# Performance work log

Measured on AMD Instinct MI355X. Metric: run time of the kernel, lower is better.

The kernel has to match this reference:

```python
import jax, jax.numpy as jnp
import numpy as np

DIM = 1024
HEADS = 16
HEAD_DIM = DIM // HEADS
HIDDEN = 4 * DIM
EPS = 1e-5

def _layernorm(x, w, b):
    mu = jnp.mean(x, axis=-1, keepdims=True)
    var = jnp.mean(jnp.square(x - mu), axis=-1, keepdims=True)
    return (x - mu) * jax.lax.rsqrt(var + EPS) * w + b

def setup_inputs() -> dict:
    key = jax.random.key(0)
    ks = jax.random.split(key, 8)
    B, N, C = 4, 1024, DIM
    s = lambda fan_in: 1.0 / np.sqrt(fan_in)
    return {
        "x": jax.random.normal(ks[0], (B, N, C), dtype=jnp.float32),
        "ln1_w": jnp.ones((C,), jnp.float32),
        "ln1_b": jnp.zeros((C,), jnp.float32),
        "qkv_w": jax.random.normal(ks[1], (3 * C, C), jnp.float32) * s(C),
        "proj_w": jax.random.normal(ks[2], (C, C), jnp.float32) * s(C),
        "proj_b": jnp.zeros((C,), jnp.float32),
        "ln2_w": jnp.ones((C,), jnp.float32),
        "ln2_b": jnp.zeros((C,), jnp.float32),
        "fc1_w": jax.random.normal(ks[3], (HIDDEN, C), jnp.float32) * s(C),
        "fc1_b": jnp.zeros((HIDDEN,), jnp.float32),
        "fc2_w": jax.random.normal(ks[4], (C, HIDDEN), jnp.float32) * s(HIDDEN),
        "fc2_b": jnp.zeros((C,), jnp.float32),
    }

def reference(x, ln1_w, ln1_b, qkv_w, proj_w, proj_b, ln2_w, ln2_b, fc1_w, fc1_b, fc2_w, fc2_b):
    B, N, C = x.shape
    H, D = HEADS, HEAD_DIM
    scale = D ** -0.5
    # --- attention branch (pre-norm) ---
    h = _layernorm(x, ln1_w, ln1_b)
    qkv = jnp.einsum('bnc,oc->bno', h, qkv_w)          # [B,N,3C], no bias (qkv_bias=False)
    qkv = qkv.reshape(B, N, 3, H, D)
    q = jnp.transpose(qkv[:, :, 0], (0, 2, 1, 3))       # [B,H,N,D]
    k = jnp.transpose(qkv[:, :, 1], (0, 2, 1, 3))
    v = jnp.transpose(qkv[:, :, 2], (0, 2, 1, 3))
    attn = jnp.einsum('bhnd,bhmd->bhnm', q, k) * scale  # [B,H,N,N]
    attn = jax.nn.softmax(attn, axis=-1)
    o = jnp.einsum('bhnm,bhmd->bhnd', attn, v)          # [B,H,N,D]
    o = jnp.transpose(o, (0, 2, 1, 3)).reshape(B, N, C)
    o = jnp.einsum('bnc,oc->bno', o, proj_w) + proj_b
    x = x + o
    # --- MLP branch (pre-norm); drop=0.0 -> identity ---
    h = _layernorm(x, ln2_w, ln2_b)
    h = jnp.einsum('bnc,hc->bnh', h, fc1_w) + fc1_b
    h = jax.nn.gelu(h, approximate=False)               # nn.GELU exact erf form
    h = jnp.einsum('bnh,ch->bnc', h, fc2_w) + fc2_b
    return x + h
```

## Files before the change

### kernel.cpp

```cpp
#include <hip/hip_runtime.h>
#include <hip/hip_bf16.h>
#include <math.h>
#include <stdint.h>

#define SEQ 1024
#define CDIM 1024
#define NHEAD 16
#define HIDDEN 4096
#define BATCH 4
#define MROWS (BATCH*SEQ)

using bf16x8 = __attribute__((ext_vector_type(8))) short;
using f32x4  = __attribute__((ext_vector_type(4))) float;

__device__ __forceinline__ short f2bf(float f) {
    union { float f; uint32_t u; } c; c.f = f;
    const uint32_t u = c.u + 0x7FFFu + ((c.u >> 16) & 1u);
    return (short)(u >> 16);
}

__device__ __forceinline__ float gelu_exact(float v) {
    return 0.5f * v * (1.0f + erff(v * 0.70710678118654752440f));
}

__device__ __forceinline__ void gload_lds16(const short* g, short* lds) {
    __builtin_amdgcn_global_load_lds(
        (const __attribute__((address_space(1))) void*)(uintptr_t)g,
        (__attribute__((address_space(3))) void*)(uintptr_t)lds,
        16, 0, 0);
}

__global__ void cvt_bf16_kernel(const float* __restrict__ in, short* __restrict__ out) {
    const size_t i = ((size_t)blockIdx.x * 256 + threadIdx.x) * 8;
    const float4 a = *(const float4*)(in + i);
    const float4 b = *(const float4*)(in + i + 4);
    bf16x8 s;
    s[0] = f2bf(a.x); s[1] = f2bf(a.y); s[2] = f2bf(a.z); s[3] = f2bf(a.w);
    s[4] = f2bf(b.x); s[5] = f2bf(b.y); s[6] = f2bf(b.z); s[7] = f2bf(b.w);
    *(bf16x8*)(out + i) = s;
}

__global__ void ln_kernel(const float* __restrict__ x, const float* __restrict__ w,
                          const float* __restrict__ b, short* __restrict__ out) {
    const int row = blockIdx.x;
    const int t = threadIdx.x;
    const float4* xr = (const float4*)(x + (size_t)row * CDIM);
    float4 v = xr[t];
    float s  = v.x + v.y + v.z + v.w;
    float sq = v.x*v.x + v.y*v.y + v.z*v.z + v.w*v.w;
    #pragma unroll
    for (int off = 32; off; off >>= 1) {
        s  += __shfl_down(s, off);
        sq += __shfl_down(sq, off);
    }
    __shared__ float ss[4], ssq[4];
    const int wid = t >> 6, lane = t & 63;
    if (lane == 0) { ss[wid] = s; ssq[wid] = sq; }
    __syncthreads();
    s  = ss[0] + ss[1] + ss[2] + ss[3];
    sq = ssq[0] + ssq[1] + ssq[2] + ssq[3];
    const float mu  = s * (1.0f / CDIM);
    const float var = sq * (1.0f / CDIM) - mu * mu;
    const float rs  = rsqrtf(var + 1e-5f);
    const float4 wv = ((const float4*)w)[t];
    const float4 bv = ((const float4*)b)[t];
    short4 o;
    o.x = f2bf((v.x - mu) * rs * wv.x + bv.x);
    o.y = f2bf((v.y - mu) * rs * wv.y + bv.y);
    o.z = f2bf((v.z - mu) * rs * wv.z + bv.z);
    o.w = f2bf((v.w - mu) * rs * wv.w + bv.w);
    *(short4*)(out + (size_t)row * CDIM + t * 4) = o;
}

template<int BN, bool BIAS, bool RES, bool GELU_, bool OUTBF16>
__global__ __launch_bounds__(256) void mgemm(
    const short* __restrict__ A, const short* __restrict__ B,
    const float* __restrict__ bias, const float* __restrict__ res,
    void* __restrict__ Cv, int M, int N, int K)
{
    constexpr int MF = (BN == 128) ? 4 : 2;
    __shared__ __align__(16) short As[3][128 * 32];
    __shared__ __align__(16) short Bs[3][BN * 32];
    const int t = threadIdx.x;
    const int w = t >> 6, l = t & 63;

    const int gx = gridDim.x;
    const int nwg = gx * gridDim.y;
    const int lid = blockIdx.y * gx + blockIdx.x;
    const int swz = (lid & 7) * (nwg >> 3) + (lid >> 3);
    const int bx = swz % gx, by = swz / gx;
    const int m0 = by * 128, n0 = bx * BN;

    const int wrow = (BN == 128) ? (w >> 1) * 64 : w * 32;
    const int wcol = (BN == 128) ? (w & 1) * 64 : 0;

    const short* agp0 = A + (size_t)(m0 + w * 32 + (l >> 2)) * K + (l & 3) * 8;
    const short* agp1 = agp0 + (size_t)16 * K;
    const short* bgp0;
    const short* bgp1 = nullptr;
    if (BN == 128) {
        bgp0 = B + (size_t)(n0 + w * 32 + (l >> 2)) * K + (l & 3) * 8;
        bgp1 = bgp0 + (size_t)16 * K;
    } else {
        bgp0 = B + (size_t)(n0 + w * 16 + (l >> 2)) * K + (l & 3) * 8;
    }

    int aoff[MF], boff[4];
    #pragma unroll
    for (int m = 0; m < MF; ++m) aoff[m] = (wrow + m * 16 + (l & 15)) * 32 + (l >> 4) * 8;
    #pragma unroll
    for (int n = 0; n < 4; ++n)  boff[n] = (wcol + n * 16 + (l & 15)) * 32 + (l >> 4) * 8;

    auto stage = [&](int k0, int buf) {
        short* ldsA = &As[buf][w * 1024];
        gload_lds16(agp0 + k0, ldsA);
        gload_lds16(agp1 + k0, ldsA + 512);
        if (BN == 128) {
            short* ldsB = &Bs[buf][w * 1024];
            gload_lds16(bgp0 + k0, ldsB);
            gload_lds16(bgp1 + k0, ldsB + 512);
        } else {
            gload_lds16(bgp0 + k0, &Bs[buf][w * 512]);
        }
    };

    f32x4 acc[MF][4] = {};
    const int T = K / 32;
    stage(0, 0);
    stage(32, 1);
    int cur = 0;
    for (int kt = 0; kt < T; ++kt) {
        if (kt < T - 1) {
            if constexpr (BN == 128) asm volatile("s_waitcnt vmcnt(4)" ::: "memory");
            else                     asm volatile("s_waitcnt vmcnt(3)" ::: "memory");
        } else {
            asm volatile("s_waitcnt vmcnt(0)" ::: "memory");
        }
        __builtin_amdgcn_sched_barrier(0);
        __builtin_amdgcn_s_barrier();
        __builtin_amdgcn_sched_barrier(0);
        if (kt + 2 < T) {
            int nb = kt + 2; nb -= (nb >= 3) ? ((nb / 3) * 3) : 0;
            stage((kt + 2) * 32, nb);
        }
        bf16x8 af[MF], bfr[4];
        #pragma unroll
        for (int m = 0; m < MF; ++m) af[m]  = *(const bf16x8*)&As[cur][aoff[m]];
        #pragma unroll
        for (int n = 0; n < 4; ++n)  bfr[n] = *(const bf16x8*)&Bs[cur][boff[n]];
        #pragma unroll
        for (int m = 0; m < MF; ++m)
            #pragma unroll
            for (int n = 0; n < 4; ++n)
                acc[m][n] = __builtin_amdgcn_mfma_f32_16x16x32_bf16(af[m], bfr[n], acc[m][n], 0, 0, 0);
        cur = (cur == 2) ? 0 : cur + 1;
    }

    const int lr4 = (l >> 4) * 4, lc = l & 15;
    #pragma unroll
    for (int m = 0; m < MF; ++m) {
        #pragma unroll
        for (int n = 0; n < 4; ++n) {
            const int col = n0 + wcol + n * 16 + lc;
            const float bv = BIAS ? bias[col] : 0.0f;
            #pragma unroll
            for (int r = 0; r < 4; ++r) {
                const int row = m0 + wrow + m * 16 + lr4 + r;
                float v = acc[m][n][r] + bv;
                if (GELU_) v = gelu_exact(v);
                if (RES)   v += res[(size_t)row * N + col];
                if (OUTBF16) ((short*)Cv)[(size_t)row * N + col] = f2bf(v);
                else         ((float*)Cv)[(size_t)row * N + col] = v;
            }
        }
    }
}

__global__ __launch_bounds__(256) void qkv_gemm(
    const short* __restrict__ A, const short* __restrict__ B,
    short* __restrict__ qkvb, short* __restrict__ VT, int K)
{
    __shared__ __align__(16) short As[3][128 * 32];
    __shared__ __align__(16) short Bs[3][128 * 32];
    const int t = threadIdx.x;
    const int w = t >> 6, l = t & 63;
    const int wr = w >> 1, wc = w & 1;

    const int gx = gridDim.x;
    const int nwg = gx * gridDim.y;
    const int lid = blockIdx.y * gx + blockIdx.x;
    const int swz = (lid & 7) * (nwg >> 3) + (lid >> 3);
    const int bx = swz % gx, by = swz / gx;
    const int m0 = by * 128, n0 = bx * 128;

    const short* agp0 = A + (size_t)(m0 + w * 32 + (l >> 2)) * K + (l & 3) * 8;
    const short* agp1 = agp0 + (size_t)16 * K;
    const short* bgp0 = B + (size_t)(n0 + w * 32 + (l >> 2)) * K + (l & 3) * 8;
    const short* bgp1 = bgp0 + (size_t)16 * K;

    int aoff[4], boff[4];
    #pragma unroll
    for (int m = 0; m < 4; ++m) aoff[m] = (wr * 64 + m * 16 + (l & 15)) * 32 + (l >> 4) * 8;
    #pragma unroll
    for (int n = 0; n < 4; ++n) boff[n] = (wc * 64 + n * 16 + (l & 15)) * 32 + (l >> 4) * 8;

    auto stage = [&](int k0, int buf) {
        short* ldsA = &As[buf][w * 1024];
        short* ldsB = &Bs[buf][w * 1024];
        gload_lds16(agp0 + k0, ldsA);
        gload_lds16(agp1 + k0, ldsA + 512);
        gload_lds16(bgp0 + k0, ldsB);
        gload_lds16(bgp1 + k0, ldsB + 512);
    };

    f32x4 acc[4][4] = {};
    const int T = K / 32;
    stage(0, 0);
    stage(32, 1);
    int cur = 0;
    for (int kt = 0; kt < T; ++kt) {
        if (kt < T - 1) asm volatile("s_waitcnt vmcnt(4)" ::: "memory");
        else            asm volatile("s_waitcnt vmcnt(0)" ::: "memory");
        __builtin_amdgcn_sched_barrier(0);
        __builtin_amdgcn_s_barrier();
        __builtin_amdgcn_sched_barrier(0);
        if (kt + 2 < T) {
            int nb = kt + 2; nb -= (nb >= 3) ? ((nb / 3) * 3) : 0;
            stage((kt + 2) * 32, nb);
        }
        bf16x8 af[4], bfr[4];
        #pragma unroll
        for (int m = 0; m < 4; ++m) af[m]  = *(const bf16x8*)&As[cur][aoff[m]];
        #pragma unroll
        for (int n = 0; n < 4; ++n) bfr[n] = *(const bf16x8*)&Bs[cur][boff[n]];
        #pragma unroll
        for (int m = 0; m < 4; ++m)
            #pragma unroll
            for (int n = 0; n < 4; ++n)
                acc[m][n] = __builtin_amdgcn_mfma_f32_16x16x32_bf16(af[m], bfr[n], acc[m][n], 0, 0, 0);
        cur = (cur == 2) ? 0 : cur + 1;
    }

    const int lr4 = (l >> 4) * 4, lc = l & 15;
    if (n0 < 2048) {
        const float sc = (n0 < 1024) ? 0.125f : 1.0f;
        #pragma unroll
        for (int m = 0; m < 4; ++m) {
            #pragma unroll
            for (int n = 0; n < 4; ++n) {
                const int col = n0 + wc * 64 + n * 16 + lc;
                #pragma unroll
                for (int r = 0; r < 4; ++r) {
                    const int row = m0 + wr * 64 + m * 16 + lr4 + r;
                    qkvb[(size_t)row * 2048 + col] = f2bf(acc[m][n][r] * sc);
                }
            }
        }
    } else {
        #pragma unroll
        for (int m = 0; m < 4; ++m) {
            const int row0 = m0 + wr * 64 + m * 16 + lr4;
            const int b = row0 >> 10, nseq = row0 & 1023;
            #pragma unroll
            for (int n = 0; n < 4; ++n) {
                const int c2 = n0 - 2048 + wc * 64 + n * 16 + lc;
                const int h = c2 >> 6, d = c2 & 63;
                short4 v4;
                v4.x = f2bf(acc[m][n][0]); v4.y = f2bf(acc[m][n][1]);
                v4.z = f2bf(acc[m][n][2]); v4.w = f2bf(acc[m][n][3]);
                *(short4*)&VT[(((size_t)(b * 16 + h) * 64 + d) * 1024) + nseq] = v4;
            }
        }
    }
}

__global__ __launch_bounds__(256) void fattn(const short* __restrict__ qkvb,
                                             const short* __restrict__ VT,
                                             short* __restrict__ o) {
    const int bh = blockIdx.y;
    const int b = bh >> 4, h = bh & 15;
    const int q0 = blockIdx.x * 64;
    const int t = threadIdx.x, w = t >> 6, l = t & 63;

    __shared__ __align__(16) short Ks[2][64 * 64];
    __shared__ __align__(16) short Vs[2][64 * 64];
    __shared__ __align__(16) short Ps[4][1024];

    const size_t qrow = (size_t)(b * SEQ + q0 + w * 16 + (l & 15)) * 2048 + h * 64;
    bf16x8 qf[2];
    qf[0] = *(const bf16x8*)&qkvb[qrow + (l >> 4) * 8];
    qf[1] = *(const bf16x8*)&qkvb[qrow + 32 + (l >> 4) * 8];

    const int srow = l >> 3;
    const int sc16 = (l & 7) ^ (srow & 7);
    const short* Kg = qkvb + 1024 + h * 64;
    const short* Vg = VT + (size_t)bh * 64 * 1024;

    f32x4 acc[4] = {};
    float mrow[4] = {-1e30f, -1e30f, -1e30f, -1e30f};
    float lrow[4] = {0.f, 0.f, 0.f, 0.f};

    auto stage = [&](int kt, int buf) {
        const int kv0 = kt * 64;
        #pragma unroll
        for (int i = 0; i < 2; ++i) {
            const int r0 = w * 16 + i * 8;
            gload_lds16(Kg + (size_t)(b * SEQ + kv0 + r0 + srow) * 2048 + sc16 * 8,
                        &Ks[buf][r0 * 64]);
            gload_lds16(Vg + (size_t)(r0 + srow) * 1024 + kv0 + sc16 * 8,
                        &Vs[buf][r0 * 64]);
        }
    };

    stage(0, 0);
    for (int kt = 0; kt < 16; ++kt) {
        const int cur = kt & 1;
        __syncthreads();
        if (kt + 1 < 16) stage(kt + 1, cur ^ 1);

        f32x4 sacc[4];
        #pragma unroll
        for (int nt = 0; nt < 4; ++nt) {
            f32x4 z = {};
            #pragma unroll
            for (int ks = 0; ks < 2; ++ks) {
                const int row = nt * 16 + (l & 15);
                const int c16 = (ks * 4 + (l >> 4)) ^ (row & 7);
                const bf16x8 kf = *(const bf16x8*)&Ks[cur][row * 64 + c16 * 8];
                z = __builtin_amdgcn_mfma_f32_16x16x32_bf16(qf[ks], kf, z, 0, 0, 0);
            }
            sacc[nt] = z;
        }
        float tmax[4], tsum[4], fac[4];
        #pragma unroll
        for (int r = 0; r < 4; ++r)
            tmax[r] = fmaxf(fmaxf(sacc[0][r], sacc[1][r]), fmaxf(sacc[2][r], sacc[3][r]));
        #pragma unroll
        for (int off = 1; off <= 8; off <<= 1)
            #pragma unroll
            for (int r = 0; r < 4; ++r)
                tmax[r] = fmaxf(tmax[r], __shfl_xor(tmax[r], off));
        #pragma unroll
        for (int r = 0; r < 4; ++r) {
            const float nm = fmaxf(mrow[r], tmax[r]);
            fac[r] = __expf(mrow[r] - nm);
            mrow[r] = nm;
            tsum[r] = 0.0f;
        }
        #pragma unroll
        for (int nt = 0; nt < 4; ++nt) {
            #pragma unroll
            for (int r = 0; r < 4; ++r) {
                const float p = __expf(sacc[nt][r] - mrow[r]);
                tsum[r] += p;
                const int q = (l >> 4) * 4 + r;
                const int kv = nt * 16 + (l & 15);
                union { float f; uint32_t u; } cu; cu.f = p;
                Ps[w][q * 64 + (kv ^ ((q & 7) << 3))] = (short)((cu.u + 0x8000u) >> 16);
            }
        }
        #pragma unroll
        for (int off = 1; off <= 8; off <<= 1)
            #pragma unroll
            for (int r = 0; r < 4; ++r)
                tsum[r] += __shfl_xor(tsum[r], off);
        #pragma unroll
        for (int r = 0; r < 4; ++r) lrow[r] = lrow[r] * fac[r] + tsum[r];
        #pragma unroll
        for (int nt2 = 0; nt2 < 4; ++nt2)
            #pragma unroll
            for (int r = 0; r < 4; ++r)
                acc[nt2][r] *= fac[r];
        #pragma unroll
        for (int ks = 0; ks < 2; ++ks) {
            const int ql = l & 15;
            const bf16x8 pa = *(const bf16x8*)&Ps[w][ql * 64 + ((ks * 32 + (l >> 4) * 8) ^ ((ql & 7) << 3))];
            #pragma unroll
            for (int nt2 = 0; nt2 < 4; ++nt2) {
                const int row = nt2 * 16 + (l & 15);
                const int c16 = (ks * 4 + (l >> 4)) ^ (row & 7);
                const bf16x8 vf = *(const bf16x8*)&Vs[cur][row * 64 + c16 * 8];
                acc[nt2] = __builtin_amdgcn_mfma_f32_16x16x32_bf16(pa, vf, acc[nt2], 0, 0, 0);
            }
        }
    }
    #pragma unroll
    for (int r = 0; r < 4; ++r) {
        const float rcp = 1.0f / lrow[r];
        const int q = q0 + w * 16 + (l >> 4) * 4 + r;
        #pragma unroll
        for (int nt2 = 0; nt2 < 4; ++nt2) {
            const int d = nt2 * 16 + (l & 15);
            o[(size_t)(b * SEQ + q) * CDIM + h * 64 + d] = f2bf(acc[nt2][r] * rcp);
        }
    }
}

extern "C" void kernel_launch(void* const* d_in, const int* in_sizes, int n_in,
                              void* d_out, int out_size, void* d_ws, size_t ws_size,
                              hipStream_t stream) {
    const float* x      = (const float*)d_in[0];
    const float* ln1_w  = (const float*)d_in[1];
    const float* ln1_b  = (const float*)d_in[2];
    const float* qkv_w  = (const float*)d_in[3];
    const float* proj_w = (const float*)d_in[4];
    const float* proj_b = (const float*)d_in[5];
    const float* ln2_w  = (const float*)d_in[6];
    const float* ln2_b  = (const float*)d_in[7];
    const float* fc1_w  = (const float*)d_in[8];
    const float* fc1_b  = (const float*)d_in[9];
    const float* fc2_w  = (const float*)d_in[10];
    const float* fc2_b  = (const float*)d_in[11];
    float* out = (float*)d_out;

    short* ws16  = (short*)d_ws;
    short* wqkv  = ws16;
    short* wproj = ws16 + 3145728;
    short* wfc1  = ws16 + 4194304;
    short* wfc2  = ws16 + 8388608;
    char*  wsb   = (char*)d_ws;
    short* qkvb  = (short*)(wsb + (size_t)24 * 1024 * 1024);
    short* VT    = (short*)(wsb + (size_t)40 * 1024 * 1024);
    short* mlp1  = (short*)(wsb + (size_t)24 * 1024 * 1024);
    short* hbuf  = (short*)(wsb + (size_t)72 * 1024 * 1024);

    cvt_bf16_kernel<<<1536, 256, 0, stream>>>(qkv_w, wqkv);
    cvt_bf16_kernel<<< 512, 256, 0, stream>>>(proj_w, wproj);
    cvt_bf16_kernel<<<2048, 256, 0, stream>>>(fc1_w, wfc1);
    cvt_bf16_kernel<<<2048, 256, 0, stream>>>(fc2_w, wfc2);

    ln_kernel<<<MROWS, 256, 0, stream>>>(x, ln1_w, ln1_b, hbuf);
    qkv_gemm<<<dim3(24, 32), 256, 0, stream>>>(hbuf, wqkv, qkvb, VT, 1024);
    fattn<<<dim3(SEQ / 64, BATCH * NHEAD), 256, 0, stream>>>(qkvb, VT, hbuf);
    mgemm<64,true,true,false,false><<<dim3(16, 32), 256, 0, stream>>>(
        hbuf, wproj, proj_b, x, out, MROWS, 1024, 1024);
    ln_kernel<<<MROWS, 256, 0, stream>>>(out, ln2_w, ln2_b, hbuf);
    mgemm<128,true,false,true,true><<<dim3(32, 32), 256, 0, stream>>>(
        hbuf, wfc1, fc1_b, nullptr, mlp1, MROWS, 4096, 1024);
    mgemm<64,true,true,false,false><<<dim3(16, 32), 256, 0, stream>>>(
        mlp1, wfc2, fc2_b, out, out, MROWS, 1024, 4096);
}
```

Measured before the change: 252.1 us.

## Add 256x256 8-wave ping-pong GEMM for fc1 and XOR-swizzle LDS layouts

```diff
diff --git a/kernel.cpp b/kernel.cpp
--- a/kernel.cpp
+++ b/kernel.cpp
@@ -72,6 +72,142 @@
     *(short4*)(out + (size_t)row * CDIM + t * 4) = o;
 }
 
+template<bool BIAS, bool RES, bool GELU_, bool OUTBF16>
+__global__ __launch_bounds__(512) void gemm8p(
+    const short* __restrict__ A, const short* __restrict__ B,
+    const float* __restrict__ bias, const float* __restrict__ res,
+    void* __restrict__ Cv, int M, int N, int K)
+{
+    __shared__ __align__(16) short As[2][256 * 64];
+    __shared__ __align__(16) short Bs[2][256 * 64];
+    const int t = threadIdx.x;
+    const int w = t >> 6, l = t & 63;
+    const int wm = w >> 2, wn = w & 3;
+
+    const int lid = blockIdx.y * gridDim.x + blockIdx.x;
+    const int xcd = lid & 7, c = lid >> 3;
+    const int by = (xcd >> 1) * 4 + (c >> 3);
+    const int bx = (xcd & 1) * 8 + (c & 7);
+    const int m0 = by * 256, n0 = bx * 256;
+
+    const int trow = t >> 3;
+    const int k8s = ((t & 7) ^ (trow & 7)) * 8;
+    const short* Ag = A + (size_t)(m0 + trow) * K + k8s;
+    const short* Bg = B + (size_t)(n0 + trow) * K + k8s;
+
+    const int fr = l & 15, g = l >> 4;
+    const int sw = fr & 7;
+    const int ak0 = (g ^ sw) * 8;
+    const int ak1 = ((4 + g) ^ sw) * 8;
+    int aoff[8], boff[4];
+    #pragma unroll
+    for (int mf = 0; mf < 8; ++mf) aoff[mf] = (wm * 128 + mf * 16 + fr) * 64;
+    #pragma unroll
+    for (int nf = 0; nf < 4; ++nf) boff[nf] = (wn * 64 + nf * 16 + fr) * 64;
+
+    f32x4 acc[8][4] = {};
+
+#define STAGE8(Gb, LDSb, kt, h)                                             \
+    {                                                                       \
+        gload_lds16((Gb) + (size_t)((h) * 128) * K + (kt) * 64,             \
+                    (LDSb) + ((h) * 128 + w * 8) * 64);                     \
+        gload_lds16((Gb) + (size_t)((h) * 128 + 64) * K + (kt) * 64,        \
+                    (LDSb) + ((h) * 128 + 64 + w * 8) * 64);                \
+    }
+
+    STAGE8(Ag, As[0], 0, 0); STAGE8(Ag, As[0], 0, 1);
+    STAGE8(Bg, Bs[0], 0, 0); STAGE8(Bg, Bs[0], 0, 1);
+    asm volatile("s_waitcnt vmcnt(0)" ::: "memory");
+    __builtin_amdgcn_s_barrier();
+
+    const int T = K / 64;
+    for (int kt = 0; kt < T; ++kt) {
+        short* curA = &As[kt & 1][0];
+        short* curB = &Bs[kt & 1][0];
+        short* nxtA = &As[(kt & 1) ^ 1][0];
+        short* nxtB = &Bs[(kt & 1) ^ 1][0];
+        const bool pre = (kt + 1 < T);
+        bf16x8 bfr[4], af[4];
+
+        if (pre) STAGE8(Ag, nxtA, kt + 1, 0);
+        #pragma unroll
+        for (int nf = 0; nf < 4; ++nf) bfr[nf] = *(const bf16x8*)&curB[boff[nf] + ak0];
+        #pragma unroll
+        for (int mf = 0; mf < 4; ++mf) af[mf] = *(const bf16x8*)&curA[aoff[mf] + ak0];
+        __builtin_amdgcn_s_barrier();
+        __builtin_amdgcn_s_setprio(1);
+        #pragma unroll
+        for (int mf = 0; mf < 4; ++mf)
+            #pragma unroll
+            for (int nf = 0; nf < 4; ++nf)
+                acc[mf][nf] = __builtin_amdgcn_mfma_f32_16x16x32_bf16(af[mf], bfr[nf], acc[mf][nf], 0, 0, 0);
+        __builtin_amdgcn_s_setprio(0);
+        __builtin_amdgcn_s_barrier();
+
+        if (pre) STAGE8(Ag, nxtA, kt + 1, 1);
+        #pragma unroll
+        for (int mf = 0; mf < 4; ++mf) af[mf] = *(const bf16x8*)&curA[aoff[4 + mf] + ak0];
+        __builtin_amdgcn_s_barrier();
+        __builtin_amdgcn_s_setprio(1);
+        #pragma unroll
+        for (int mf = 0; mf < 4; ++mf)
+            #pragma unroll
+            for (int nf = 0; nf < 4; ++nf)
+                acc[4 + mf][nf] = __builtin_amdgcn_mfma_f32_16x16x32_bf16(af[mf], bfr[nf], acc[4 + mf][nf], 0, 0, 0);
+        __builtin_amdgcn_s_setprio(0);
+        __builtin_amdgcn_s_barrier();
+
+        if (pre) STAGE8(Bg, nxtB, kt + 1, 0);
+        #pragma unroll
+        for (int nf = 0; nf < 4; ++nf) bfr[nf] = *(const bf16x8*)&curB[boff[nf] + ak1];
+        #pragma unroll
+        for (int mf = 0; mf < 4; ++mf) af[mf] = *(const bf16x8*)&curA[aoff[mf] + ak1];
+        __builtin_amdgcn_s_barrier();
+        __builtin_amdgcn_s_setprio(1);
+        #pragma unroll
+        for (int mf = 0; mf < 4; ++mf)
+            #pragma unroll
+            for (int nf = 0; nf < 4; ++nf)
+                acc[mf][nf] = __builtin_amdgcn_mfma_f32_16x16x32_bf16(af[mf], bfr[nf], acc[mf][nf], 0, 0, 0);
+        __builtin_amdgcn_s_setprio(0);
+        __builtin_amdgcn_s_barrier();
+
+        if (pre) STAGE8(Bg, nxtB, kt + 1, 1);
+        #pragma unroll
+        for (int mf = 0; mf < 4; ++mf) af[mf] = *(const bf16x8*)&curA[aoff[4 + mf] + ak1];
+        __builtin_amdgcn_s_barrier();
+        __builtin_amdgcn_s_setprio(1);
+        #pragma unroll
+        for (int mf = 0; mf < 4; ++mf)
+            #pragma unroll
+            for (int nf = 0; nf < 4; ++nf)
+                acc[4 + mf][nf] = __builtin_amdgcn_mfma_f32_16x16x32_bf16(af[mf], bfr[nf], acc[4 + mf][nf], 0, 0, 0);
+        __builtin_amdgcn_s_setprio(0);
+        asm volatile("s_waitcnt vmcnt(0)" ::: "memory");
+        __builtin_amdgcn_s_barrier();
+    }
+#undef STAGE8
+
+    const int lr4 = (l >> 4) * 4, lc = l & 15;
+    #pragma unroll
+    for (int mf = 0; mf < 8; ++mf) {
+        #pragma unroll
+        for (int nf = 0; nf < 4; ++nf) {
+            const int col = n0 + wn * 64 + nf * 16 + lc;
+            const float bv = BIAS ? bias[col] : 0.0f;
+            #pragma unroll
+            for (int r = 0; r < 4; ++r) {
+                const int row = m0 + wm * 128 + mf * 16 + lr4 + r;
+                float v = acc[mf][nf][r] + bv;
+                if (GELU_) v = gelu_exact(v);
+                if (RES)   v += res[(size_t)row * N + col];
+                if (OUTBF16) ((short*)Cv)[(size_t)row * N + col] = f2bf(v);
+                else         ((float*)Cv)[(size_t)row * N + col] = v;
+            }
+        }
+    }
+}
+
 template<int BN, bool BIAS, bool RES, bool GELU_, bool OUTBF16>
 __global__ __launch_bounds__(256) void mgemm(
     const short* __restrict__ A, const short* __restrict__ B,
@@ -87,29 +223,32 @@
     const int gx = gridDim.x;
     const int nwg = gx * gridDim.y;
     const int lid = blockIdx.y * gx + blockIdx.x;
-    const int swz = (lid & 7) * (nwg >> 3) + (lid >> 3);
-    const int bx = swz % gx, by = swz / gx;
+    const int swzb = (lid & 7) * (nwg >> 3) + (lid >> 3);
+    const int bx = swzb % gx, by = swzb / gx;
     const int m0 = by * 128, n0 = bx * BN;
 
     const int wrow = (BN == 128) ? (w >> 1) * 64 : w * 32;
     const int wcol = (BN == 128) ? (w & 1) * 64 : 0;
 
-    const short* agp0 = A + (size_t)(m0 + w * 32 + (l >> 2)) * K + (l & 3) * 8;
+    const int sk8 = ((l & 3) ^ ((l >> 3) & 3)) * 8;
+    const short* agp0 = A + (size_t)(m0 + w * 32 + (l >> 2)) * K + sk8;
     const short* agp1 = agp0 + (size_t)16 * K;
     const short* bgp0;
     const short* bgp1 = nullptr;
     if (BN == 128) {
-        bgp0 = B + (size_t)(n0 + w * 32 + (l >> 2)) * K + (l & 3) * 8;
+        bgp0 = B + (size_t)(n0 + w * 32 + (l >> 2)) * K + sk8;
         bgp1 = bgp0 + (size_t)16 * K;
     } else {
-        bgp0 = B + (size_t)(n0 + w * 16 + (l >> 2)) * K + (l & 3) * 8;
-    }
-
+        bgp0 = B + (size_t)(n0 + w * 16 + (l >> 2)) * K + sk8;
+    }
+
+    const int fr = l & 15;
+    const int rsw = (fr >> 1) & 3;
     int aoff[MF], boff[4];
     #pragma unroll
-    for (int m = 0; m < MF; ++m) aoff[m] = (wrow + m * 16 + (l & 15)) * 32 + (l >> 4) * 8;
-    #pragma unroll
-    for (int n = 0; n < 4; ++n)  boff[n] = (wcol + n * 16 + (l & 15)) * 32 + (l >> 4) * 8;
+    for (int m = 0; m < MF; ++m) aoff[m] = (wrow + m * 16 + fr) * 32 + ((l >> 4) ^ rsw) * 8;
+    #pragma unroll
+    for (int n = 0; n < 4; ++n)  boff[n] = (wcol + n * 16 + fr) * 32 + ((l >> 4) ^ rsw) * 8;
 
     auto stage = [&](int k0, int buf) {
         short* ldsA = &As[buf][w * 1024];
@@ -189,20 +328,23 @@
     const int gx = gridDim.x;
     const int nwg = gx * gridDim.y;
     const int lid = blockIdx.y * gx + blockIdx.x;
-    const int swz = (lid & 7) * (nwg >> 3) + (lid >> 3);
-    const int bx = swz % gx, by = swz / gx;
+    const int swzb = (lid & 7) * (nwg >> 3) + (lid >> 3);
+    const int bx = swzb % gx, by = swzb / gx;
     const int m0 = by * 128, n0 = bx * 128;
 
-    const short* agp0 = A + (size_t)(m0 + w * 32 + (l >> 2)) * K + (l & 3) * 8;
+    const int sk8 = ((l & 3) ^ ((l >> 3) & 3)) * 8;
+    const short* agp0 = A + (size_t)(m0 + w * 32 + (l >> 2)) * K + sk8;
     const short* agp1 = agp0 + (size_t)16 * K;
-    const short* bgp0 = B + (size_t)(n0 + w * 32 + (l >> 2)) * K + (l & 3) * 8;
+    const short* bgp0 = B + (size_t)(n0 + w * 32 + (l >> 2)) * K + sk8;
     const short* bgp1 = bgp0 + (size_t)16 * K;
 
+    const int fr = l & 15;
+    const int rsw = (fr >> 1) & 3;
     int aoff[4], boff[4];
     #pragma unroll
-    for (int m = 0; m < 4; ++m) aoff[m] = (wr * 64 + m * 16 + (l & 15)) * 32 + (l >> 4) * 8;
-    #pragma unroll
-    for (int n = 0; n < 4; ++n) boff[n] = (wc * 64 + n * 16 + (l & 15)) * 32 + (l >> 4) * 8;
+    for (int m = 0; m < 4; ++m) aoff[m] = (wr * 64 + m * 16 + fr) * 32 + ((l >> 4) ^ rsw) * 8;
+    #pragma unroll
+    for (int n = 0; n < 4; ++n) boff[n] = (wc * 64 + n * 16 + fr) * 32 + ((l >> 4) ^ rsw) * 8;
 
     auto stage = [&](int k0, int buf) {
         short* ldsA = &As[buf][w * 1024];
@@ -435,7 +577,7 @@
     mgemm<64,true,true,false,false><<<dim3(16, 32), 256, 0, stream>>>(
         hbuf, wproj, proj_b, x, out, MROWS, 1024, 1024);
     ln_kernel<<<MROWS, 256, 0, stream>>>(out, ln2_w, ln2_b, hbuf);
-    mgemm<128,true,false,true,true><<<dim3(32, 32), 256, 0, stream>>>(
+    gemm8p<true,false,true,true><<<dim3(16, 16), 512, 0, stream>>>(
         hbuf, wfc1, fc1_b, nullptr, mlp1, MROWS, 4096, 1024);
     mgemm<64,true,true,false,false><<<dim3(16, 32), 256, 0, stream>>>(
         mlp1, wfc2, fc2_b, out, out, MROWS, 1024, 4096);
```

New measurement: 247.3 us. About the same (-1.9%).
